# Optimization experiments

Measured on AMD Instinct MI355X. Metric: run time of the kernel, lower is better.

Reference implementation:

```python
import jax, jax.numpy as jnp
import numpy as np

B, L, D, H, E = 64, 128, 768, 2, 131072  # graphs, nodes/graph, hidden, heads, edges
N = B * L
C = D // H  # per-head channels


def _transformer_conv(x, src, dst, wq, bq, wk, bk, wv, bv, ws, bs):
    # PyG TransformerConv (concat=True, root_weight=True, beta=False)
    n = x.shape[0]
    q = (x @ wq + bq).reshape(n, H, C)
    k = (x @ wk + bk).reshape(n, H, C)
    v = (x @ wv + bv).reshape(n, H, C)
    # per-edge attention logits [E, H]
    logits = jnp.sum(q[dst] * k[src], axis=-1) * (1.0 / np.sqrt(C))
    # scatter softmax over incoming edges of each dst node
    m = jax.ops.segment_max(logits, dst, num_segments=n)
    e = jnp.exp(logits - m[dst])
    s = jax.ops.segment_sum(e, dst, num_segments=n)
    alpha = e / s[dst]  # [E, H]
    msg = alpha[..., None] * v[src]  # [E, H, C]
    agg = jax.ops.segment_sum(msg, dst, num_segments=n).reshape(n, D)
    return agg + x @ ws + bs


def setup_inputs() -> dict:
    key = jax.random.key(0)
    ks = jax.random.split(key, 24)
    x = jax.random.normal(ks[0], (N, D), jnp.float32)
    # within-graph random edges
    dst = jax.random.randint(ks[1], (E,), 0, N)
    off = jax.random.randint(ks[2], (E,), 0, L)
    src = (dst // L) * L + off
    edge_index = jnp.stack([src, dst]).astype(jnp.int32)

    def lin(k, i, o):
        return jax.random.normal(k, (i, o), jnp.float32) * 0.02

    inp = {"x": x, "edge_index": edge_index}
    i = 3
    for layer in ("1", "2"):
        for nm in ("wq", "wk", "wv", "ws"):
            inp[nm + layer] = lin(ks[i], D, D); i += 1
            inp["b" + nm[1] + layer] = jnp.zeros((D,), jnp.float32)
    inp["atti_w"] = lin(ks[i], 2 * D, D); i += 1
    inp["atti_b"] = jnp.zeros((D,), jnp.float32)
    inp["atts_w"] = lin(ks[i], D, 1); i += 1
    inp["atts_b"] = jnp.zeros((1,), jnp.float32)
    inp["fc1_w"] = lin(ks[i], D, D); i += 1
    inp["fc1_b"] = jnp.zeros((D,), jnp.float32)
    inp["fc2_w"] = lin(ks[i], D, 3); i += 1
    inp["fc2_b"] = jnp.zeros((3,), jnp.float32)
    return inp


def reference(x, edge_index, wq1, bq1, wk1, bk1, wv1, bv1, ws1, bs1,
              wq2, bq2, wk2, bk2, wv2, bv2, ws2, bs2,
              atti_w, atti_b, atts_w, atts_b, fc1_w, fc1_b, fc2_w, fc2_b):
    src, dst = edge_index[0], edge_index[1]
    h = jax.nn.relu(_transformer_conv(x, src, dst, wq1, bq1, wk1, bk1, wv1, bv1, ws1, bs1))
    h = jax.nn.relu(_transformer_conv(h, src, dst, wq2, bq2, wk2, bk2, wv2, bv2, ws2, bs2))
    # pad(): equal-size graphs -> reshape, mask all-valid (x_mask all False)
    hp = h.reshape(B, L, D)
    # attention pooling (eval path): query = first node of each graph
    x_q = jnp.broadcast_to(hp[:, :1], hp.shape)  # [B, L, D]
    x_c = jax.nn.relu(jnp.concatenate([x_q, hp], axis=-1) @ atti_w + atti_b)
    score = x_c @ atts_w + atts_b  # [B, L, 1]
    score = jax.nn.softmax(score, axis=1)
    pooled = jnp.sum(hp * score, axis=1)  # [B, D]
    out = jnp.tanh(pooled @ fc1_w + fc1_b) @ fc2_w + fc2_b
    return jax.nn.log_softmax(out, axis=-1)
```

## Files before the change

### kernel.cpp

```cpp
#include <hip/hip_runtime.h>

#define NN 8192
#define DD 768
#define EE 131072
#define BBg 64
#define LLn 128
#define CCh 384

typedef unsigned short u16;
typedef unsigned char u8;
typedef __attribute__((ext_vector_type(8))) short short8;
typedef __attribute__((ext_vector_type(4))) float f32x4;

__device__ __forceinline__ float b2f(u16 u) {
    union { unsigned int i; float f; } x; x.i = ((unsigned int)u) << 16; return x.f;
}
__device__ __forceinline__ u16 f2b(float f) {
    union { float f; unsigned int i; } x; x.f = f;
    unsigned int r = x.i + 0x7fffu + ((x.i >> 16) & 1u);
    return (u16)(r >> 16);
}
__device__ __forceinline__ void gload16(const void* g, void* l) {
    __builtin_amdgcn_global_load_lds((const __attribute__((address_space(1))) void*)g,
                                     (__attribute__((address_space(3))) void*)l, 16, 0, 0);
}

__global__ __launch_bounds__(256) void prep_kernel(const float* __restrict__ in,
                                                   u16* __restrict__ out,
                                                   unsigned int* __restrict__ cnt32,
                                                   float* __restrict__ score) {
    int i = blockIdx.x * 256 + threadIdx.x;
    float4 v = ((const float4*)in)[i];
    ushort4 o; o.x = f2b(v.x); o.y = f2b(v.y); o.z = f2b(v.z); o.w = f2b(v.w);
    ((ushort4*)out)[i] = o;
    if (blockIdx.x < 1024) cnt32[i] = 0;
    else if (blockIdx.x < 1056) score[i - 1024 * 256] = 0.f;
}

struct TP { const float* src; u16* dst; int rowOff; };
struct TP11 { TP a[11]; };

__global__ __launch_bounds__(256) void combo_kernel(TP11 args,
                                                    const int* __restrict__ srcp,
                                                    const int* __restrict__ dstp,
                                                    unsigned int* __restrict__ cnt32) {
    __shared__ float tile[64][65];
    if (blockIdx.z == 11) {
        for (int e = blockIdx.x * 256 + threadIdx.x; e < EE; e += 144 * 256) {
            int d = dstp[e], s = srcp[e];
            int g = d >> 7;
            int idx = (g << 14) + ((d & 127) << 7) + (s & 127);
            atomicAdd(&cnt32[idx >> 2], 1u << ((idx & 3) * 8));
        }
        return;
    }
    TP tp = args.a[blockIdx.z];
    int bx = blockIdx.x % 12, by = blockIdx.x / 12;
    int n0 = bx * 64, k0 = by * 64;
    int t = threadIdx.x;
    int tc = t & 63, tr = t >> 6;
#pragma unroll
    for (int i = 0; i < 16; i++)
        tile[tr + i * 4][tc] = tp.src[(size_t)(tp.rowOff + k0 + tr + i * 4) * DD + n0 + tc];
    __syncthreads();
#pragma unroll
    for (int i = 0; i < 16; i++) {
        int row = tr + i * 4;
        tp.dst[(size_t)(n0 + row) * DD + k0 + tc] = f2b(tile[tc][row]);
    }
}

enum { EPI_F32 = 1, EPI_TANH = 3 };

__global__ __launch_bounds__(256) void gemm_bf16(const u16* __restrict__ A,
                                                 const u16* __restrict__ Wt,
                                                 const float* __restrict__ bias,
                                                 void* __restrict__ outp, int K, int mode) {
    __shared__ u16 As[64][72];
    __shared__ u16 Bs[64][72];
    const int m0 = blockIdx.y * 64, n0 = blockIdx.x * 64;
    const int t = threadIdx.x;
    const int lane = t & 63, w = t >> 6;
    const int tr = t >> 2, tc = (t & 3) * 16;
    f32x4 acc[4] = {{0,0,0,0},{0,0,0,0},{0,0,0,0},{0,0,0,0}};
    const int fRow = lane & 15;
    const int fK = (lane >> 4) * 8;

    for (int k0 = 0; k0 < K; k0 += 64) {
        int4 a0 = *(const int4*)(A + (size_t)(m0 + tr) * K + k0 + tc);
        int4 a1 = *(const int4*)(A + (size_t)(m0 + tr) * K + k0 + tc + 8);
        int4 b0 = *(const int4*)(Wt + (size_t)(n0 + tr) * K + k0 + tc);
        int4 b1 = *(const int4*)(Wt + (size_t)(n0 + tr) * K + k0 + tc + 8);
        __syncthreads();
        *(int4*)&As[tr][tc] = a0; *(int4*)&As[tr][tc + 8] = a1;
        *(int4*)&Bs[tr][tc] = b0; *(int4*)&Bs[tr][tc + 8] = b1;
        __syncthreads();
#pragma unroll
        for (int s = 0; s < 2; s++) {
            short8 af = *(const short8*)&As[w * 16 + fRow][s * 32 + fK];
#pragma unroll
            for (int g = 0; g < 4; g++) {
                short8 bf = *(const short8*)&Bs[g * 16 + fRow][s * 32 + fK];
                acc[g] = __builtin_amdgcn_mfma_f32_16x16x32_bf16(af, bf, acc[g], 0, 0, 0);
            }
        }
    }
    const int colLocal = lane & 15;
    const int rowLocal = (lane >> 4) * 4;
#pragma unroll
    for (int g = 0; g < 4; g++) {
        int col = n0 + g * 16 + colLocal;
        float bv = bias ? bias[col] : 0.f;
#pragma unroll
        for (int i = 0; i < 4; i++) {
            int row = m0 + w * 16 + rowLocal + i;
            float v = acc[g][i] + bv;
            if (mode == EPI_TANH) v = tanhf(v);
            ((float*)outp)[(size_t)row * DD + col] = v;
        }
    }
}

__global__ __launch_bounds__(256, 2) void gemm256(const u16* __restrict__ A,
                                                  const u16* __restrict__ Wt,
                                                  const float* __restrict__ b0,
                                                  const float* __restrict__ b1,
                                                  const float* __restrict__ b2,
                                                  const float* __restrict__ b3,
                                                  u16* __restrict__ o0, u16* __restrict__ o1,
                                                  u16* __restrict__ o2, u16* __restrict__ o3) {
    __shared__ u16 smem[256 * 64 + 128 * 64];
    u16* As = smem;
    u16* Bs = smem + 256 * 64;
    const int K = DD;
    const int t = threadIdx.x;
    const int lane = t & 63, w = t >> 6;
    const int wr = w >> 1, wc = w & 1;
    const int m0 = blockIdx.y * 256, n0 = blockIdx.x * 128;
    const int fRow = lane & 15, fThr = lane >> 4;
    f32x4 acc[8][4] = {};
    const u16* Abase = A + (size_t)m0 * K;
    const u16* Bbase = Wt + (size_t)n0 * K;

    for (int k0 = 0; k0 < K; k0 += 64) {
        __syncthreads();
#pragma unroll
        for (int i = 0; i < 8; i++) {
            int c = t + 256 * i;
            int row = c >> 3;
            int col = ((c & 7) ^ (row & 7)) * 8;
            gload16(Abase + (size_t)row * K + k0 + col, (char*)As + (size_t)c * 16);
        }
#pragma unroll
        for (int i = 0; i < 4; i++) {
            int c = t + 256 * i;
            int row = c >> 3;
            int col = ((c & 7) ^ (row & 7)) * 8;
            gload16(Bbase + (size_t)row * K + k0 + col, (char*)Bs + (size_t)c * 16);
        }
        __syncthreads();
#pragma unroll
        for (int kk = 0; kk < 64; kk += 32) {
            const int cjW = (kk >> 3) + fThr;
            short8 af[8], bf[4];
#pragma unroll
            for (int i = 0; i < 8; i++) {
                int R = wr * 128 + i * 16 + fRow;
                af[i] = *(const short8*)&As[(R * 8 + (cjW ^ (R & 7))) * 8];
            }
#pragma unroll
            for (int g = 0; g < 4; g++) {
                int R = wc * 64 + g * 16 + fRow;
                bf[g] = *(const short8*)&Bs[(R * 8 + (cjW ^ (R & 7))) * 8];
            }
#pragma unroll
            for (int i = 0; i < 8; i++)
#pragma unroll
                for (int g = 0; g < 4; g++)
                    acc[i][g] = __builtin_amdgcn_mfma_f32_16x16x32_bf16(af[i], bf[g], acc[i][g], 0, 0, 0);
        }
    }
    const int chunk = n0 / DD;
    const float* bp = (chunk == 0) ? b0 : (chunk == 1) ? b1 : (chunk == 2) ? b2 : b3;
    u16* op = (chunk == 0) ? o0 : (chunk == 1) ? o1 : (chunk == 2) ? o2 : o3;
    const int cb0 = n0 - chunk * DD;
    if (chunk == 2) {
        u16 (*Cs2)[264] = (u16(*)[264])smem;
#pragma unroll
        for (int p = 0; p < 2; p++) {
            __syncthreads();
            if (wc == p) {
#pragma unroll
                for (int g = 0; g < 4; g++) {
                    float bv = bp[cb0 + p * 64 + g * 16 + fRow];
#pragma unroll
                    for (int i = 0; i < 8; i++)
#pragma unroll
                        for (int rr = 0; rr < 4; rr++)
                            Cs2[g * 16 + fRow][wr * 128 + i * 16 + fThr * 4 + rr] =
                                f2b(acc[i][g][rr] + bv);
                }
            }
            __syncthreads();
#pragma unroll
            for (int ii = 0; ii < 16; ii++) {
                int c = t + 256 * ii;
                int col = c >> 6, ch = c & 63;
                *(ushort4*)(op + (size_t)(cb0 + p * 64 + col) * NN + m0 + ch * 4) =
                    *(const ushort4*)&Cs2[col][ch * 4];
            }
        }
    } else {
        u16 (*Cs)[136] = (u16(*)[136])smem;
#pragma unroll
        for (int p = 0; p < 2; p++) {
            __syncthreads();
            if (wr == p) {
#pragma unroll
                for (int g = 0; g < 4; g++) {
                    float bv = bp[cb0 + wc * 64 + g * 16 + fRow];
#pragma unroll
                    for (int i = 0; i < 8; i++)
#pragma unroll
                        for (int rr = 0; rr < 4; rr++)
                            Cs[i * 16 + fThr * 4 + rr][wc * 64 + g * 16 + fRow] =
                                f2b(acc[i][g][rr] + bv);
                }
            }
            __syncthreads();
#pragma unroll
            for (int ii = 0; ii < 16; ii++) {
                int c = t + 256 * ii;
                int row = c >> 5, ch = c & 31;
                *(ushort4*)(op + (size_t)(m0 + p * 128 + row) * DD + cb0 + ch * 4) =
                    *(const ushort4*)&Cs[row][ch * 4];
            }
        }
    }
}

__global__ __launch_bounds__(256) void gemm_xc(const u16* __restrict__ A,
                                               const u16* __restrict__ Wt,
                                               const u16* __restrict__ wt8,
                                               const float* __restrict__ atti_b,
                                               const float* __restrict__ atts_w,
                                               float* __restrict__ score) {
    __shared__ u16 As[128 * 64];
    __shared__ u16 Bs[128 * 64];
    __shared__ float aq_p[2][128];
    const int K = DD;
    const int t = threadIdx.x;
    const int lane = t & 63, w = t >> 6;
    const int wr = w >> 1, wc = w & 1;
    const int n0 = blockIdx.x * 128, m0 = blockIdx.y * 128;
    const int fRow = lane & 15, fThr = lane >> 4;

    {
        int col = t & 127, kh = t >> 7;
        const u16* xr = A + (size_t)m0 * DD + kh * 384;
        const u16* wr8 = wt8 + (size_t)(n0 + col) * DD + kh * 384;
        float s = 0.f;
#pragma unroll 8
        for (int j = 0; j < 96; j++) {
            ushort4 a4 = *(const ushort4*)(xr + j * 4);
            ushort4 b4 = *(const ushort4*)(wr8 + j * 4);
            s += b2f(a4.x) * b2f(b4.x) + b2f(a4.y) * b2f(b4.y)
               + b2f(a4.z) * b2f(b4.z) + b2f(a4.w) * b2f(b4.w);
        }
        aq_p[kh][col] = s;
    }

    f32x4 acc[4][4] = {};
    const u16* Abase = A + (size_t)m0 * K;
    const u16* Bbase = Wt + (size_t)n0 * K;
    for (int k0 = 0; k0 < K; k0 += 64) {
        __syncthreads();
#pragma unroll
        for (int i = 0; i < 4; i++) {
            int c = t + 256 * i;
            int row = c >> 3;
            int col = ((c & 7) ^ (row & 7)) * 8;
            gload16(Abase + (size_t)row * K + k0 + col, (char*)As + (size_t)c * 16);
            gload16(Bbase + (size_t)row * K + k0 + col, (char*)Bs + (size_t)c * 16);
        }
        __syncthreads();
#pragma unroll
        for (int kk = 0; kk < 64; kk += 32) {
            const int cjW = (kk >> 3) + fThr;
            short8 af[4], bf[4];
#pragma unroll
            for (int i = 0; i < 4; i++) {
                int R = wr * 64 + i * 16 + fRow;
                af[i] = *(const short8*)&As[(R * 8 + (cjW ^ (R & 7))) * 8];
            }
#pragma unroll
            for (int g = 0; g < 4; g++) {
                int R = wc * 64 + g * 16 + fRow;
                bf[g] = *(const short8*)&Bs[(R * 8 + (cjW ^ (R & 7))) * 8];
            }
#pragma unroll
            for (int i = 0; i < 4; i++)
#pragma unroll
                for (int g = 0; g < 4; g++)
                    acc[i][g] = __builtin_amdgcn_mfma_f32_16x16x32_bf16(af[i], bf[g], acc[i][g], 0, 0, 0);
        }
    }
    float rsum[4][4] = {};
#pragma unroll
    for (int g = 0; g < 4; g++) {
        int cl = wc * 64 + g * 16 + fRow;
        int col = n0 + cl;
        float bv = atti_b[col] + aq_p[0][cl] + aq_p[1][cl];
        float av = atts_w[col];
#pragma unroll
        for (int i = 0; i < 4; i++)
#pragma unroll
            for (int rr = 0; rr < 4; rr++) {
                float v = fmaxf(acc[i][g][rr] + bv, 0.f);
                rsum[i][rr] += v * av;
            }
    }
#pragma unroll
    for (int i = 0; i < 4; i++)
#pragma unroll
        for (int rr = 0; rr < 4; rr++) {
            float s = rsum[i][rr];
            s += __shfl_xor(s, 1, 16); s += __shfl_xor(s, 2, 16);
            s += __shfl_xor(s, 4, 16); s += __shfl_xor(s, 8, 16);
            if (fRow == 0)
                atomicAdd(&score[m0 + wr * 64 + i * 16 + fThr * 4 + rr], s);
        }
}

__global__ __launch_bounds__(256) void attn_fused(const u16* __restrict__ qb,
                                                  const u16* __restrict__ kb,
                                                  const u16* __restrict__ vT,
                                                  const u8* __restrict__ cnt,
                                                  const u16* __restrict__ hs,
                                                  u16* __restrict__ out) {
    __shared__ u16 As[64][72];
    __shared__ u16 Bs[128][72];
    __shared__ u16 Pl[64][136];
    __shared__ u16 Vt[64][136];
    const int half = blockIdx.x, hd = blockIdx.y, g = blockIdx.z;
    const int t = threadIdx.x;
    const int lane = t & 63, w = t >> 6;
    const int fRow = lane & 15, fThr = lane >> 4;
    const int dstBase = g * 128 + half * 64;
    const u16* Qb = qb + (size_t)dstBase * DD + hd * CCh;
    const u16* Kb = kb + (size_t)(g * 128) * DD + hd * CCh;

    f32x4 acc[8] = {};
    const int trA = t >> 2, tcA = (t & 3) * 16;
    const int trB = t >> 1, tcB = (t & 1) * 32;
    for (int k0 = 0; k0 < CCh; k0 += 64) {
        int4 a0 = *(const int4*)(Qb + (size_t)trA * DD + k0 + tcA);
        int4 a1 = *(const int4*)(Qb + (size_t)trA * DD + k0 + tcA + 8);
        int4 b0 = *(const int4*)(Kb + (size_t)trB * DD + k0 + tcB);
        int4 b1 = *(const int4*)(Kb + (size_t)trB * DD + k0 + tcB + 8);
        int4 b2 = *(const int4*)(Kb + (size_t)trB * DD + k0 + tcB + 16);
        int4 b3 = *(const int4*)(Kb + (size_t)trB * DD + k0 + tcB + 24);
        __syncthreads();
        *(int4*)&As[trA][tcA] = a0; *(int4*)&As[trA][tcA + 8] = a1;
        *(int4*)&Bs[trB][tcB] = b0; *(int4*)&Bs[trB][tcB + 8] = b1;
        *(int4*)&Bs[trB][tcB + 16] = b2; *(int4*)&Bs[trB][tcB + 24] = b3;
        __syncthreads();
#pragma unroll
        for (int kk = 0; kk < 64; kk += 32) {
            short8 af = *(const short8*)&As[w * 16 + fRow][kk + fThr * 8];
#pragma unroll
            for (int j = 0; j < 8; j++) {
                short8 bf = *(const short8*)&Bs[j * 16 + fRow][kk + fThr * 8];
                acc[j] = __builtin_amdgcn_mfma_f32_16x16x32_bf16(af, bf, acc[j], 0, 0, 0);
            }
        }
    }

    const float scale = 0.05103103630798288f;
    const u8* cg = cnt + ((size_t)g << 14);
    const int rbase = half * 64 + w * 16 + fThr * 4;
    float pv[8][4];
#pragma unroll
    for (int i = 0; i < 4; i++) {
        float m = -3.4e38f;
#pragma unroll
        for (int j = 0; j < 8; j++) {
            float c = (float)cg[(rbase + i) * 128 + j * 16 + fRow];
            float s = acc[j][i] * scale;
            pv[j][i] = c;
            if (c > 0.f) m = fmaxf(m, s);
        }
#pragma unroll
        for (int msk = 1; msk <= 8; msk <<= 1) m = fmaxf(m, __shfl_xor(m, msk, 16));
        float sum = 0.f;
#pragma unroll
        for (int j = 0; j < 8; j++) {
            float p = (pv[j][i] > 0.f) ? pv[j][i] * __expf(acc[j][i] * scale - m) : 0.f;
            pv[j][i] = p; sum += p;
        }
#pragma unroll
        for (int msk = 1; msk <= 8; msk <<= 1) sum += __shfl_xor(sum, msk, 16);
        float inv = (sum > 0.f) ? 1.f / sum : 0.f;
#pragma unroll
        for (int j = 0; j < 8; j++)
            Pl[w * 16 + fThr * 4 + i][j * 16 + fRow] = f2b(pv[j][i] * inv);
    }

    for (int cc = 0; cc < 6; cc++) {
        __syncthreads();
#pragma unroll
        for (int ii = 0; ii < 4; ii++) {
            int q = t + 256 * ii;
            int row = q >> 4, col = (q & 15) * 8;
            *(int4*)&Vt[row][col] =
                *(const int4*)(vT + (size_t)(hd * CCh + cc * 64 + row) * NN + g * 128 + col);
        }
        __syncthreads();
        f32x4 acc2[4] = {};
#pragma unroll
        for (int kk = 0; kk < 128; kk += 32) {
            short8 af = *(const short8*)&Pl[w * 16 + fRow][kk + fThr * 8];
#pragma unroll
            for (int j = 0; j < 4; j++) {
                short8 bf = *(const short8*)&Vt[j * 16 + fRow][kk + fThr * 8];
                acc2[j] = __builtin_amdgcn_mfma_f32_16x16x32_bf16(af, bf, acc2[j], 0, 0, 0);
            }
        }
#pragma unroll
        for (int j = 0; j < 4; j++) {
            int c = hd * CCh + cc * 64 + j * 16 + fRow;
#pragma unroll
            for (int i = 0; i < 4; i++) {
                int row = dstBase + w * 16 + fThr * 4 + i;
                size_t idx = (size_t)row * DD + c;
                float r = fmaxf(acc2[j][i] + b2f(hs[idx]), 0.f);
                out[idx] = f2b(r);
            }
        }
    }
}

__global__ __launch_bounds__(192) void pool_kernel(const float* __restrict__ score,
                                                   const u16* __restrict__ hx,
                                                   u16* __restrict__ pb) {
    int b = blockIdx.x, t = threadIdx.x;
    __shared__ float sprob[LLn];
    if (t < 64) {
        float s0 = score[b * LLn + t];
        float s1 = score[b * LLn + 64 + t];
        float mx = fmaxf(s0, s1);
#pragma unroll
        for (int m = 1; m <= 32; m <<= 1) mx = fmaxf(mx, __shfl_xor(mx, m, 64));
        float e0 = __expf(s0 - mx), e1 = __expf(s1 - mx);
        float sum = e0 + e1;
#pragma unroll
        for (int m = 1; m <= 32; m <<= 1) sum += __shfl_xor(sum, m, 64);
        float inv = 1.f / sum;
        sprob[t] = e0 * inv; sprob[t + 64] = e1 * inv;
    }
    __syncthreads();
    int c = t * 4;
    float a0 = 0, a1 = 0, a2 = 0, a3 = 0;
    for (int l = 0; l < LLn; l++) {
        float wl = sprob[l];
        ushort4 hv = *(const ushort4*)(hx + (size_t)(b * LLn + l) * DD + c);
        a0 += wl * b2f(hv.x); a1 += wl * b2f(hv.y); a2 += wl * b2f(hv.z); a3 += wl * b2f(hv.w);
    }
    ushort4 o; o.x = f2b(a0); o.y = f2b(a1); o.z = f2b(a2); o.w = f2b(a3);
    *(ushort4*)(pb + (size_t)b * DD + c) = o;
}

__global__ __launch_bounds__(256) void head2_kernel(const float* __restrict__ u,
                                                    const float* __restrict__ fc2w,
                                                    const float* __restrict__ fc2b,
                                                    float* __restrict__ outp) {
    int b = blockIdx.x, t = threadIdx.x;
    __shared__ float sred[4][3];
    float p0 = 0, p1 = 0, p2 = 0;
    for (int k = t; k < DD; k += 256) {
        float uv = u[(size_t)b * DD + k];
        p0 += uv * fc2w[k * 3 + 0]; p1 += uv * fc2w[k * 3 + 1]; p2 += uv * fc2w[k * 3 + 2];
    }
#pragma unroll
    for (int m = 1; m <= 32; m <<= 1) {
        p0 += __shfl_xor(p0, m, 64); p1 += __shfl_xor(p1, m, 64); p2 += __shfl_xor(p2, m, 64);
    }
    int w = t >> 6, lane = t & 63;
    if (lane == 0) { sred[w][0] = p0; sred[w][1] = p1; sred[w][2] = p2; }
    __syncthreads();
    if (t == 0) {
        float z0 = fc2b[0], z1 = fc2b[1], z2 = fc2b[2];
        for (int i = 0; i < 4; i++) { z0 += sred[i][0]; z1 += sred[i][1]; z2 += sred[i][2]; }
        float mx = fmaxf(z0, fmaxf(z1, z2));
        float lse = mx + logf(__expf(z0 - mx) + __expf(z1 - mx) + __expf(z2 - mx));
        outp[b * 3 + 0] = z0 - lse; outp[b * 3 + 1] = z1 - lse; outp[b * 3 + 2] = z2 - lse;
    }
}

static inline char* carve(char*& p, size_t bytes) {
    char* r = p;
    p += (bytes + 255) & ~(size_t)255;
    return r;
}

extern "C" void kernel_launch(void* const* d_in, const int* in_sizes, int n_in,
                              void* d_out, int out_size, void* d_ws, size_t ws_size,
                              hipStream_t stream) {
    const float* x = (const float*)d_in[0];
    const int* ei = (const int*)d_in[1];
    const int* srcp = ei;
    const int* dstp = ei + EE;
    const float* wL[8] = {(const float*)d_in[2], (const float*)d_in[4], (const float*)d_in[6],
                          (const float*)d_in[8], (const float*)d_in[10], (const float*)d_in[12],
                          (const float*)d_in[14], (const float*)d_in[16]};
    const float* bL[8] = {(const float*)d_in[3], (const float*)d_in[5], (const float*)d_in[7],
                          (const float*)d_in[9], (const float*)d_in[11], (const float*)d_in[13],
                          (const float*)d_in[15], (const float*)d_in[17]};
    const float* atti_w = (const float*)d_in[18];
    const float* atti_b = (const float*)d_in[19];
    const float* atts_w = (const float*)d_in[20];
    const float* fc1_w = (const float*)d_in[22];
    const float* fc1_b = (const float*)d_in[23];
    const float* fc2_w = (const float*)d_in[24];
    const float* fc2_b = (const float*)d_in[25];
    float* outp = (float*)d_out;

    char* p = (char*)d_ws;
    const size_t ndb = (size_t)NN * DD * 2;
    const size_t wsz = (size_t)DD * DD * 2;
    u16* qb = (u16*)carve(p, ndb);
    u16* kb = (u16*)carve(p, ndb);
    u16* vt = (u16*)carve(p, ndb);
    u16* xb = (u16*)carve(p, ndb);
    u16* hb = (u16*)carve(p, ndb);
    u16* hs = (u16*)carve(p, ndb);
    u16* wtcat1 = (u16*)carve(p, wsz * 4);
    u16* wtcat2 = (u16*)carve(p, wsz * 4);
    u16* wt8 = (u16*)carve(p, wsz);
    u16* wt9 = (u16*)carve(p, wsz);
    u16* wtfc1 = (u16*)carve(p, wsz);
    u16* pb = (u16*)carve(p, (size_t)BBg * DD * 2);
    float* uu = (float*)carve(p, (size_t)BBg * DD * 4);
    u8* cnt = (u8*)carve(p, (size_t)BBg * 128 * 128);
    float* score = (float*)carve(p, NN * 4);

    prep_kernel<<<6144, 256, 0, stream>>>(x, xb, (unsigned int*)cnt, score);

    TP11 tps;
    for (int i = 0; i < 4; i++) tps.a[i] = {wL[i], wtcat1 + (size_t)i * DD * DD, 0};
    for (int i = 0; i < 4; i++) tps.a[4 + i] = {wL[4 + i], wtcat2 + (size_t)i * DD * DD, 0};
    tps.a[8] = {atti_w, wt8, 0};
    tps.a[9] = {atti_w, wt9, DD};
    tps.a[10] = {fc1_w, wtfc1, 0};
    combo_kernel<<<dim3(144, 1, 12), 256, 0, stream>>>(tps, srcp, dstp, (unsigned int*)cnt);

    dim3 gf(24, 32);
    dim3 ga(2, 2, BBg);
    gemm256<<<gf, 256, 0, stream>>>(xb, wtcat1, bL[0], bL[1], bL[2], bL[3], qb, kb, vt, hs);
    attn_fused<<<ga, 256, 0, stream>>>(qb, kb, vt, cnt, hs, hb);
    gemm256<<<gf, 256, 0, stream>>>(hb, wtcat2, bL[4], bL[5], bL[6], bL[7], qb, kb, vt, hs);
    attn_fused<<<ga, 256, 0, stream>>>(qb, kb, vt, cnt, hs, xb);

    gemm_xc<<<dim3(6, 64), 256, 0, stream>>>(xb, wt9, wt8, atti_b, atts_w, score);

    pool_kernel<<<BBg, 192, 0, stream>>>(score, xb, pb);
    gemm_bf16<<<dim3(12, 1), 256, 0, stream>>>(pb, wtfc1, fc1_b, uu, DD, EPI_TANH);
    head2_kernel<<<BBg, 256, 0, stream>>>(uu, fc2_w, fc2_b, outp);
}
```

Before: 347.4 us.

## Triple-buffer gemm256 K-loop with 512 threads and split prefetch/MFMA phases

Rewrites the fused QKVS projection GEMM to use 512 threads (8 waves, 4x2 wave grid with 64x64 per-wave tiles) and a three-slab LDS ring. Global-to-LDS loads for tile k+2 are issued in two halves interleaved with two MFMA phases, with explicit vmcnt waits, raw barriers and s_setprio around the MFMA blocks. The aim is to hide global load latency behind compute and cut per-wave register pressure. In exchange it uses more LDS per block, which may lower occupancy, and the hand-placed waitcnt and barrier synchronisation is fragile.

```diff
diff --git a/kernel.cpp b/kernel.cpp
--- a/kernel.cpp
+++ b/kernel.cpp
@@ -121,7 +121,8 @@
     }
 }
 
-__global__ __launch_bounds__(256, 2) void gemm256(const u16* __restrict__ A,
+#define SLAB 24576
+__global__ __launch_bounds__(512, 2) void gemm256(const u16* __restrict__ A,
                                                   const u16* __restrict__ Wt,
                                                   const float* __restrict__ b0,
                                                   const float* __restrict__ b1,
@@ -129,112 +130,153 @@
                                                   const float* __restrict__ b3,
                                                   u16* __restrict__ o0, u16* __restrict__ o1,
                                                   u16* __restrict__ o2, u16* __restrict__ o3) {
-    __shared__ u16 smem[256 * 64 + 128 * 64];
-    u16* As = smem;
-    u16* Bs = smem + 256 * 64;
+    __shared__ u16 smem[3 * SLAB];
     const int K = DD;
     const int t = threadIdx.x;
     const int lane = t & 63, w = t >> 6;
     const int wr = w >> 1, wc = w & 1;
     const int m0 = blockIdx.y * 256, n0 = blockIdx.x * 128;
     const int fRow = lane & 15, fThr = lane >> 4;
-    f32x4 acc[8][4] = {};
     const u16* Abase = A + (size_t)m0 * K;
     const u16* Bbase = Wt + (size_t)n0 * K;
 
-    for (int k0 = 0; k0 < K; k0 += 64) {
-        __syncthreads();
-#pragma unroll
-        for (int i = 0; i < 8; i++) {
-            int c = t + 256 * i;
+    auto stage = [&](u16* slab, int kt2, int j) {
+        const int k0 = kt2 * 64;
+        if (j < 4) {
+            int c = t + 512 * j;
             int row = c >> 3;
             int col = ((c & 7) ^ (row & 7)) * 8;
-            gload16(Abase + (size_t)row * K + k0 + col, (char*)As + (size_t)c * 16);
-        }
-#pragma unroll
-        for (int i = 0; i < 4; i++) {
-            int c = t + 256 * i;
+            gload16(Abase + (size_t)row * K + k0 + col, (char*)slab + (size_t)c * 16);
+        } else {
+            int c = t + 512 * (j - 4);
             int row = c >> 3;
             int col = ((c & 7) ^ (row & 7)) * 8;
-            gload16(Bbase + (size_t)row * K + k0 + col, (char*)Bs + (size_t)c * 16);
-        }
-        __syncthreads();
-#pragma unroll
-        for (int kk = 0; kk < 64; kk += 32) {
-            const int cjW = (kk >> 3) + fThr;
-            short8 af[8], bf[4];
-#pragma unroll
-            for (int i = 0; i < 8; i++) {
-                int R = wr * 128 + i * 16 + fRow;
-                af[i] = *(const short8*)&As[(R * 8 + (cjW ^ (R & 7))) * 8];
-            }
-#pragma unroll
-            for (int g = 0; g < 4; g++) {
-                int R = wc * 64 + g * 16 + fRow;
-                bf[g] = *(const short8*)&Bs[(R * 8 + (cjW ^ (R & 7))) * 8];
-            }
-#pragma unroll
-            for (int i = 0; i < 8; i++)
-#pragma unroll
-                for (int g = 0; g < 4; g++)
-                    acc[i][g] = __builtin_amdgcn_mfma_f32_16x16x32_bf16(af[i], bf[g], acc[i][g], 0, 0, 0);
-        }
-    }
+            gload16(Bbase + (size_t)row * K + k0 + col, (char*)(slab + 16384) + (size_t)c * 16);
+        }
+    };
+
+#pragma unroll
+    for (int j = 0; j < 6; ++j) stage(smem, 0, j);
+#pragma unroll
+    for (int j = 0; j < 6; ++j) stage(smem + SLAB, 1, j);
+    asm volatile("s_waitcnt vmcnt(6)" ::: "memory");
+    __builtin_amdgcn_s_barrier();
+
+    f32x4 acc[4][4] = {};
+    int cur = 0;
+    for (int kt = 0; kt < 12; ++kt) {
+        const u16* As = smem + cur * SLAB;
+        const u16* Bs = As + 16384;
+        int nx = cur + 2; if (nx >= 3) nx -= 3;
+        u16* slabN = smem + nx * SLAB;
+        const bool pf = (kt < 10);
+
+        short8 af[4][2];
+#pragma unroll
+        for (int kk2 = 0; kk2 < 2; ++kk2) {
+            const int cj = kk2 * 4 + fThr;
+#pragma unroll
+            for (int i = 0; i < 4; ++i) {
+                const int R = wr * 64 + i * 16 + fRow;
+                af[i][kk2] = *(const short8*)&As[((size_t)R * 8 + (cj ^ (R & 7))) * 8];
+            }
+        }
+        short8 bfA[2][2];
+#pragma unroll
+        for (int kk2 = 0; kk2 < 2; ++kk2) {
+            const int cj = kk2 * 4 + fThr;
+#pragma unroll
+            for (int g = 0; g < 2; ++g) {
+                const int Rb = wc * 64 + g * 16 + fRow;
+                bfA[g][kk2] = *(const short8*)&Bs[((size_t)Rb * 8 + (cj ^ (Rb & 7))) * 8];
+            }
+        }
+        if (pf) { stage(slabN, kt + 2, 0); stage(slabN, kt + 2, 1); stage(slabN, kt + 2, 2); }
+        __builtin_amdgcn_s_barrier();
+        asm volatile("s_waitcnt lgkmcnt(0)" ::: "memory");
+        __builtin_amdgcn_s_setprio(1);
+#pragma unroll
+        for (int kk2 = 0; kk2 < 2; ++kk2)
+#pragma unroll
+            for (int i = 0; i < 4; ++i)
+#pragma unroll
+                for (int g = 0; g < 2; ++g)
+                    acc[i][g] = __builtin_amdgcn_mfma_f32_16x16x32_bf16(af[i][kk2], bfA[g][kk2],
+                                                                        acc[i][g], 0, 0, 0);
+        __builtin_amdgcn_s_setprio(0);
+        __builtin_amdgcn_s_barrier();
+        short8 bfB[2][2];
+#pragma unroll
+        for (int kk2 = 0; kk2 < 2; ++kk2) {
+            const int cj = kk2 * 4 + fThr;
+#pragma unroll
+            for (int g = 0; g < 2; ++g) {
+                const int Rb = wc * 64 + (g + 2) * 16 + fRow;
+                bfB[g][kk2] = *(const short8*)&Bs[((size_t)Rb * 8 + (cj ^ (Rb & 7))) * 8];
+            }
+        }
+        if (pf) { stage(slabN, kt + 2, 3); stage(slabN, kt + 2, 4); stage(slabN, kt + 2, 5); }
+        __builtin_amdgcn_s_barrier();
+        asm volatile("s_waitcnt lgkmcnt(0)" ::: "memory");
+        __builtin_amdgcn_s_setprio(1);
+#pragma unroll
+        for (int kk2 = 0; kk2 < 2; ++kk2)
+#pragma unroll
+            for (int i = 0; i < 4; ++i)
+#pragma unroll
+                for (int g = 0; g < 2; ++g)
+                    acc[i][g + 2] = __builtin_amdgcn_mfma_f32_16x16x32_bf16(af[i][kk2], bfB[g][kk2],
+                                                                            acc[i][g + 2], 0, 0, 0);
+        __builtin_amdgcn_s_setprio(0);
+        if (kt < 10) asm volatile("s_waitcnt vmcnt(6)" ::: "memory");
+        else if (kt == 10) asm volatile("s_waitcnt vmcnt(0)" ::: "memory");
+        __builtin_amdgcn_s_barrier();
+        cur += 1; if (cur == 3) cur = 0;
+    }
+
     const int chunk = n0 / DD;
     const float* bp = (chunk == 0) ? b0 : (chunk == 1) ? b1 : (chunk == 2) ? b2 : b3;
     u16* op = (chunk == 0) ? o0 : (chunk == 1) ? o1 : (chunk == 2) ? o2 : o3;
     const int cb0 = n0 - chunk * DD;
     if (chunk == 2) {
-        u16 (*Cs2)[264] = (u16(*)[264])smem;
-#pragma unroll
-        for (int p = 0; p < 2; p++) {
-            __syncthreads();
-            if (wc == p) {
-#pragma unroll
-                for (int g = 0; g < 4; g++) {
-                    float bv = bp[cb0 + p * 64 + g * 16 + fRow];
-#pragma unroll
-                    for (int i = 0; i < 8; i++)
-#pragma unroll
-                        for (int rr = 0; rr < 4; rr++)
-                            Cs2[g * 16 + fRow][wr * 128 + i * 16 + fThr * 4 + rr] =
-                                f2b(acc[i][g][rr] + bv);
-                }
-            }
-            __syncthreads();
-#pragma unroll
-            for (int ii = 0; ii < 16; ii++) {
-                int c = t + 256 * ii;
-                int col = c >> 6, ch = c & 63;
-                *(ushort4*)(op + (size_t)(cb0 + p * 64 + col) * NN + m0 + ch * 4) =
-                    *(const ushort4*)&Cs2[col][ch * 4];
-            }
+        u16 (*Vt)[264] = (u16(*)[264])smem;
+#pragma unroll
+        for (int g = 0; g < 4; g++) {
+            float bv = bp[cb0 + wc * 64 + g * 16 + fRow];
+#pragma unroll
+            for (int i = 0; i < 4; i++)
+#pragma unroll
+                for (int rr = 0; rr < 4; rr++)
+                    Vt[wc * 64 + g * 16 + fRow][wr * 64 + i * 16 + fThr * 4 + rr] =
+                        f2b(acc[i][g][rr] + bv);
+        }
+        __syncthreads();
+#pragma unroll
+        for (int ii = 0; ii < 16; ii++) {
+            int c = t + 512 * ii;
+            int col = c >> 6, ch = c & 63;
+            *(ushort4*)(op + (size_t)(cb0 + col) * NN + m0 + ch * 4) =
+                *(const ushort4*)&Vt[col][ch * 4];
         }
     } else {
         u16 (*Cs)[136] = (u16(*)[136])smem;
 #pragma unroll
-        for (int p = 0; p < 2; p++) {
-            __syncthreads();
-            if (wr == p) {
-#pragma unroll
-                for (int g = 0; g < 4; g++) {
-                    float bv = bp[cb0 + wc * 64 + g * 16 + fRow];
-#pragma unroll
-                    for (int i = 0; i < 8; i++)
-#pragma unroll
-                        for (int rr = 0; rr < 4; rr++)
-                            Cs[i * 16 + fThr * 4 + rr][wc * 64 + g * 16 + fRow] =
-                                f2b(acc[i][g][rr] + bv);
-                }
-            }
-            __syncthreads();
-#pragma unroll
-            for (int ii = 0; ii < 16; ii++) {
-                int c = t + 256 * ii;
-                int row = c >> 5, ch = c & 31;
-                *(ushort4*)(op + (size_t)(m0 + p * 128 + row) * DD + cb0 + ch * 4) =
-                    *(const ushort4*)&Cs[row][ch * 4];
-            }
+        for (int g = 0; g < 4; g++) {
+            float bv = bp[cb0 + wc * 64 + g * 16 + fRow];
+#pragma unroll
+            for (int i = 0; i < 4; i++)
+#pragma unroll
+                for (int rr = 0; rr < 4; rr++)
+                    Cs[wr * 64 + i * 16 + fThr * 4 + rr][wc * 64 + g * 16 + fRow] =
+                        f2b(acc[i][g][rr] + bv);
+        }
+        __syncthreads();
+#pragma unroll
+        for (int ii = 0; ii < 16; ii++) {
+            int c = t + 512 * ii;
+            int row = c >> 5, ch = c & 31;
+            *(ushort4*)(op + (size_t)(m0 + row) * DD + cb0 + ch * 4) =
+                *(const ushort4*)&Cs[row][ch * 4];
         }
     }
 }
@@ -556,9 +598,9 @@
 
     dim3 gf(24, 32);
     dim3 ga(2, 2, BBg);
-    gemm256<<<gf, 256, 0, stream>>>(xb, wtcat1, bL[0], bL[1], bL[2], bL[3], qb, kb, vt, hs);
+    gemm256<<<gf, 512, 0, stream>>>(xb, wtcat1, bL[0], bL[1], bL[2], bL[3], qb, kb, vt, hs);
     attn_fused<<<ga, 256, 0, stream>>>(qb, kb, vt, cnt, hs, hb);
-    gemm256<<<gf, 256, 0, stream>>>(hb, wtcat2, bL[4], bL[5], bL[6], bL[7], qb, kb, vt, hs);
+    gemm256<<<gf, 512, 0, stream>>>(hb, wtcat2, bL[4], bL[5], bL[6], bL[7], qb, kb, vt, hs);
     attn_fused<<<ga, 256, 0, stream>>>(qb, kb, vt, cnt, hs, xb);
 
     gemm_xc<<<dim3(6, 64), 256, 0, stream>>>(xb, wt9, wt8, atti_b, atts_w, score);
```

New measurement: 329.6 us. 1.05x faster.
